# Kernel optimization log

Measured on AMD Instinct MI355X. Metric: run time of the kernel, lower is better.

Reference implementation:

```python
import jax, jax.numpy as jnp
import numpy as np

B, NQ, NV, DIM, HEADS, K = 2, 2048, 2048, 256, 8, 8
HD = DIM // HEADS
HID = 4 * DIM
SCALE = HD ** -0.5
EPS = 1e-5


def setup_inputs() -> dict:
    key = jax.random.key(0)
    ks = jax.random.split(key, 40)
    r = lambda i, s: jax.random.normal(ks[i], s, jnp.float32) * 0.02
    inp = {
        'q': jax.random.normal(ks[0], (B, NQ, DIM), jnp.float32),
        'v': jax.random.normal(ks[1], (B, NV, DIM), jnp.float32),
        'q_pos': jax.random.normal(ks[2], (B, NQ, 3), jnp.float32),
        'v_pos': jax.random.normal(ks[3], (B, NV, 3), jnp.float32),
        'self_knn_index': jax.random.randint(ks[4], (B, NQ, K), 0, NQ, jnp.int32),
        'cross_knn_index': jax.random.randint(ks[5], (B, NQ, K), 0, NV, jnp.int32),
        # LayerNorms (gamma=1, beta=0)
        'norm1_g': jnp.ones(DIM), 'norm1_b': jnp.zeros(DIM),
        'normq_g': jnp.ones(DIM), 'normq_b': jnp.zeros(DIM),
        'normv_g': jnp.ones(DIM), 'normv_b': jnp.zeros(DIM),
        'norm2_g': jnp.ones(DIM), 'norm2_b': jnp.zeros(DIM),
        # self-attention (qkv_bias=False), proj has bias
        'sa_qkv_w': r(6, (DIM, 3 * DIM)),
        'sa_proj_w': r(7, (DIM, DIM)), 'sa_proj_b': jnp.zeros(DIM),
        # cross-attention: q proj and kv proj (no bias), out proj with bias
        'ca_q_w': r(8, (DIM, DIM)),
        'ca_kv_w': r(9, (DIM, 2 * DIM)),
        'ca_proj_w': r(10, (DIM, DIM)), 'ca_proj_b': jnp.zeros(DIM),
        # MLP
        'fc1_w': r(11, (DIM, HID)), 'fc1_b': jnp.zeros(HID),
        'fc2_w': r(12, (HID, DIM)), 'fc2_b': jnp.zeros(DIM),
        # kNN maps
        'knn_w': r(13, (2 * DIM, DIM)), 'knn_b': jnp.zeros(DIM),
        'merge_w': r(14, (2 * DIM, DIM)), 'merge_b': jnp.zeros(DIM),
        'knnx_w': r(15, (2 * DIM, DIM)), 'knnx_b': jnp.zeros(DIM),
        'mergex_w': r(16, (2 * DIM, DIM)), 'mergex_b': jnp.zeros(DIM),
    }
    return inp


def _ln(x, g, b):
    m = x.mean(-1, keepdims=True)
    var = x.var(-1, keepdims=True)
    return (x - m) / jnp.sqrt(var + EPS) * g + b


def _heads(x):  # [B,N,DIM] -> [B,H,N,HD]
    Bx, N, _ = x.shape
    return x.reshape(Bx, N, HEADS, HD).transpose(0, 2, 1, 3)


def _attend(qh, kh, vh, proj_w, proj_b):
    a = jax.nn.softmax(jnp.einsum('bhqd,bhkd->bhqk', qh, kh) * SCALE, axis=-1)
    o = jnp.einsum('bhqk,bhkd->bhqd', a, vh)
    Bx, _, N, _ = o.shape
    o = o.transpose(0, 2, 1, 3).reshape(Bx, N, DIM)
    return o @ proj_w + proj_b


_gather = jax.vmap(lambda pts, idx: pts[idx])  # ([N,D],[Nq,K]) -> [Nq,K,D]


def _knn_feature(qn, vn, idx):  # gather -> diff/cat -> [B,Nq,K,2D]
    local = _gather(vn, idx)                      # [B,Nq,K,D]
    qe = qn[:, :, None, :]                        # [B,Nq,1,D]
    return jnp.concatenate([local - qe, jnp.broadcast_to(qe, local.shape)], -1)


def reference(q, v, q_pos, v_pos, self_knn_index, cross_knn_index,
              norm1_g, norm1_b, normq_g, normq_b, normv_g, normv_b,
              norm2_g, norm2_b, sa_qkv_w, sa_proj_w, sa_proj_b,
              ca_q_w, ca_kv_w, ca_proj_w, ca_proj_b,
              fc1_w, fc1_b, fc2_w, fc2_b,
              knn_w, knn_b, merge_w, merge_b,
              knnx_w, knnx_b, mergex_w, mergex_b):
    # ---- self-attention block with self-kNN branch ----
    nq = _ln(q, norm1_g, norm1_b)
    qkv = nq @ sa_qkv_w
    qh, kh, vh = (_heads(t) for t in jnp.split(qkv, 3, axis=-1))
    sa_out = _attend(qh, kh, vh, sa_proj_w, sa_proj_b)
    f = _knn_feature(nq, nq, self_knn_index)
    knn_out = jax.nn.leaky_relu(f @ knn_w + knn_b, 0.2).max(axis=-2)
    q1 = jnp.concatenate([sa_out, knn_out], -1) @ merge_w + merge_b
    q = q + q1
    # ---- cross-attention block with cross-kNN branch ----
    nq2 = _ln(q, normq_g, normq_b)
    nv = _ln(v, normv_g, normv_b)
    qh = _heads(nq2 @ ca_q_w)
    kh, vh = (_heads(t) for t in jnp.split(nv @ ca_kv_w, 2, axis=-1))
    ca_out = _attend(qh, kh, vh, ca_proj_w, ca_proj_b)
    f = _knn_feature(nq2, nv, cross_knn_index)
    knnx_out = jax.nn.leaky_relu(f @ knnx_w + knnx_b, 0.2).max(axis=-2)
    q2 = jnp.concatenate([ca_out, knnx_out], -1) @ mergex_w + mergex_b
    q = q + q2
    # ---- MLP block ----
    h = _ln(q, norm2_g, norm2_b)
    h = jax.nn.gelu(h @ fc1_w + fc1_b, approximate=False)
    q = q + (h @ fc2_w + fc2_b)
    return q
```

## Files before the change

### kernel.cpp

```cpp
#include <hip/hip_runtime.h>
#include <math.h>

#define NQC   2048
#define NKVC  2048
#define DIMC  256
#define SCALEF 0.2550348810731232f

typedef short bfrag __attribute__((ext_vector_type(8)));
typedef float ffrag __attribute__((ext_vector_type(4)));
typedef unsigned short us8 __attribute__((ext_vector_type(8)));

__device__ __forceinline__ float gelu_exact(float x) {
    return 0.5f * x * (1.0f + erff(x * 0.70710678118654752f));
}
__device__ __forceinline__ unsigned short f2bf(float f) {
    union { float f; unsigned u; } v; v.f = f;
    unsigned r = v.u + 0x7FFFu + ((v.u >> 16) & 1u);
    return (unsigned short)(r >> 16);
}
__device__ __forceinline__ float bf2f(unsigned short u) {
    union { unsigned u; float f; } v; v.u = ((unsigned)u) << 16;
    return v.f;
}
__device__ __forceinline__ float fexp2(float x) {
    float r; asm("v_exp_f32 %0, %1" : "=v"(r) : "v"(x)); return r;
}
__device__ __forceinline__ unsigned cvt_pk_bf16(float lo, float hi) {
    unsigned r; asm("v_cvt_pk_bf16_f32 %0, %1, %2" : "=v"(r) : "v"(lo), "v"(hi));
    return r;
}

__device__ __forceinline__ void ln_row(
    const float* __restrict__ x, const float* __restrict__ g,
    const float* __restrict__ b, unsigned short* __restrict__ y, int row)
{
    int lane = threadIdx.x & 63;
    const float* xr = x + (size_t)row * DIMC + lane * 4;
    float4 vv = *(const float4*)xr;
    float s  = vv.x + vv.y + vv.z + vv.w;
    float sq = vv.x*vv.x + vv.y*vv.y + vv.z*vv.z + vv.w*vv.w;
    #pragma unroll
    for (int off = 32; off >= 1; off >>= 1) {
        s  += __shfl_xor(s, off);
        sq += __shfl_xor(sq, off);
    }
    float mean = s * (1.0f/DIMC);
    float inv  = rsqrtf(sq * (1.0f/DIMC) - mean*mean + 1e-5f);
    float4 gg = *(const float4*)(g + lane*4);
    float4 bb = *(const float4*)(b + lane*4);
    ushort4 o;
    o.x = f2bf((vv.x - mean) * inv * gg.x + bb.x);
    o.y = f2bf((vv.y - mean) * inv * gg.y + bb.y);
    o.z = f2bf((vv.z - mean) * inv * gg.z + bb.z);
    o.w = f2bf((vv.w - mean) * inv * gg.w + bb.w);
    *(ushort4*)(y + (size_t)row * DIMC + lane * 4) = o;
}

__global__ __launch_bounds__(256) void prep_ln(
    const float* __restrict__ qkv, const float* __restrict__ knn,
    const float* __restrict__ proj, const float* __restrict__ merge,
    const float* __restrict__ caq, const float* __restrict__ knnx,
    const float* __restrict__ cakv, const float* __restrict__ projx,
    const float* __restrict__ mergex, const float* __restrict__ fc1,
    const float* __restrict__ fc2, unsigned short* __restrict__ dst,
    const float* __restrict__ lx, const float* __restrict__ lg,
    const float* __restrict__ lb, unsigned short* __restrict__ ly,
    const float* __restrict__ vx, const float* __restrict__ vg,
    const float* __restrict__ vb, unsigned short* __restrict__ vy,
    const float* __restrict__ pb1, const float* __restrict__ mb1, float* __restrict__ bf1o,
    const float* __restrict__ pbx, const float* __restrict__ mbx, float* __restrict__ bfxo)
{
    if (blockIdx.x >= 3584) {
        const float* bp = (blockIdx.x == 3584) ? pb1 : pbx;
        const float* Wm = (blockIdx.x == 3584) ? merge : mergex;
        const float* bm = (blockIdx.x == 3584) ? mb1 : mbx;
        float* o        = (blockIdx.x == 3584) ? bf1o : bfxo;
        int m = threadIdx.x;
        float acc = bm[m];
        for (int k = 0; k < 256; ++k) acc += bp[k] * Wm[(size_t)k * 256 + m];
        o[m] = acc;
        return;
    }
    if (blockIdx.x >= 2560) {
        int row = (blockIdx.x - 2560) * 4 + (threadIdx.x >> 6);
        ln_row(vx, vg, vb, vy, row);
        return;
    }
    if (blockIdx.x >= 1536) {
        int row = (blockIdx.x - 1536) * 4 + (threadIdx.x >> 6);
        ln_row(lx, lg, lb, ly, row);
        return;
    }
    int e = (blockIdx.x * 256 + threadIdx.x) * 4;
    float v[4];
    float scale = 1.0f;
    if (e < 327680) {
        int n = e >> 8, k = e & 255;
        if (n < 768) {
            const float* s = qkv + (size_t)k * 768 + n;
            #pragma unroll
            for (int i = 0; i < 4; ++i) v[i] = s[(size_t)i * 768];
            if (n < 256) scale = SCALEF;
        } else if (n < 1024) {
            const float* s = knn + (size_t)k * 256 + (n - 768);
            #pragma unroll
            for (int i = 0; i < 4; ++i) v[i] = s[(size_t)i * 256];
        } else {
            const float* s = knn + (size_t)k * 256 + (n - 1024);
            #pragma unroll
            for (int i = 0; i < 4; ++i) v[i] = s[65536 + (size_t)i * 256] - s[(size_t)i * 256];
        }
    } else if (e < 393216) {
        int l = e - 327680;
        const float* s = proj + l;
        #pragma unroll
        for (int i = 0; i < 4; ++i) v[i] = s[i];
    } else if (e < 524288) {
        int l = e - 393216, n = l >> 9, k = l & 511;
        const float* s = merge + (size_t)k * 256 + n;
        #pragma unroll
        for (int i = 0; i < 4; ++i) v[i] = s[(size_t)i * 256];
    } else if (e < 655360) {
        int l = e - 524288, n = l >> 8, k = l & 255;
        if (n < 256) {
            const float* s = caq + (size_t)k * 256 + n;
            #pragma unroll
            for (int i = 0; i < 4; ++i) v[i] = s[(size_t)i * 256];
            scale = SCALEF;
        } else {
            const float* s = knnx + (size_t)k * 256 + (n - 256);
            #pragma unroll
            for (int i = 0; i < 4; ++i) v[i] = s[65536 + (size_t)i * 256] - s[(size_t)i * 256];
        }
    } else if (e < 851968) {
        int l = e - 655360, n = l >> 8, k = l & 255;
        if (n < 512) {
            const float* s = cakv + (size_t)k * 512 + n;
            #pragma unroll
            for (int i = 0; i < 4; ++i) v[i] = s[(size_t)i * 512];
        } else {
            const float* s = knnx + (size_t)k * 256 + (n - 512);
            #pragma unroll
            for (int i = 0; i < 4; ++i) v[i] = s[(size_t)i * 256];
        }
    } else if (e < 917504) {
        int l = e - 851968;
        const float* s = projx + l;
        #pragma unroll
        for (int i = 0; i < 4; ++i) v[i] = s[i];
    } else if (e < 1048576) {
        int l = e - 917504, n = l >> 9, k = l & 511;
        const float* s = mergex + (size_t)k * 256 + n;
        #pragma unroll
        for (int i = 0; i < 4; ++i) v[i] = s[(size_t)i * 256];
    } else if (e < 1310720) {
        int l = e - 1048576, n = l >> 8, k = l & 255;
        const float* s = fc1 + (size_t)k * 1024 + n;
        #pragma unroll
        for (int i = 0; i < 4; ++i) v[i] = s[(size_t)i * 1024];
    } else {
        int l = e - 1310720, n = l >> 10, k = l & 1023;
        const float* s = fc2 + (size_t)k * 256 + n;
        #pragma unroll
        for (int i = 0; i < 4; ++i) v[i] = s[(size_t)i * 256];
    }
    ushort4 o;
    o.x = f2bf(v[0] * scale); o.y = f2bf(v[1] * scale);
    o.z = f2bf(v[2] * scale); o.w = f2bf(v[3] * scale);
    *(ushort4*)(dst + e) = o;
}

__global__ __launch_bounds__(256) void ln_b(
    const float* __restrict__ x, const float* __restrict__ g,
    const float* __restrict__ b, unsigned short* __restrict__ y)
{
    ln_row(x, g, b, y, blockIdx.x * 4 + (threadIdx.x >> 6));
}

template<int ACT, int RESID, int OUTBF, int VTM>
__device__ __forceinline__ void gemm_body(
    const unsigned short* __restrict__ A, int lda,
    const unsigned short* __restrict__ Wt,
    const float* __restrict__ bias,
    const float* __restrict__ resid, int ldr,
    void* __restrict__ Cp, int ldc, int Kc, int row0, int col0,
    unsigned short (* __restrict__ Alds)[72],
    unsigned short (* __restrict__ Wlds)[72],
    unsigned short* __restrict__ vt, int vlo)
{
    const int tid = threadIdx.x;
    const int wid = tid >> 6, lane = tid & 63;
    const int lm = lane & 15, quad = lane >> 4;
    const int wr = wid >> 1, wc = wid & 1;
    const int ar = tid >> 2, ac = (tid & 3) * 16;
    const unsigned short* Ag = A  + (size_t)(row0 + ar) * lda + ac;
    const unsigned short* Wg = Wt + (size_t)(col0 + ar) * Kc  + ac;

    us8 a0 = *(const us8*)Ag;
    us8 a1 = *(const us8*)(Ag + 8);
    us8 w0 = *(const us8*)Wg;
    us8 w1 = *(const us8*)(Wg + 8);

    ffrag acc[2][2];
    #pragma unroll
    for (int mi = 0; mi < 2; ++mi)
        #pragma unroll
        for (int ni = 0; ni < 2; ++ni)
            acc[mi][ni] = (ffrag){0.f, 0.f, 0.f, 0.f};

    for (int k0 = 0;;) {
        __syncthreads();
        *(us8*)&Alds[ar][ac]   = a0;
        *(us8*)&Alds[ar][ac+8] = a1;
        *(us8*)&Wlds[ar][ac]   = w0;
        *(us8*)&Wlds[ar][ac+8] = w1;
        __syncthreads();
        k0 += 64;
        if (k0 < Kc) {
            a0 = *(const us8*)(Ag + k0);
            a1 = *(const us8*)(Ag + k0 + 8);
            w0 = *(const us8*)(Wg + k0);
            w1 = *(const us8*)(Wg + k0 + 8);
        }
        #pragma unroll
        for (int kc = 0; kc < 2; ++kc) {
            bfrag af[2], bw[2];
            #pragma unroll
            for (int mi = 0; mi < 2; ++mi)
                af[mi] = *(const bfrag*)&Alds[wr*32 + mi*16 + lm][kc*32 + quad*8];
            #pragma unroll
            for (int ni = 0; ni < 2; ++ni)
                bw[ni] = *(const bfrag*)&Wlds[wc*32 + ni*16 + lm][kc*32 + quad*8];
            #pragma unroll
            for (int mi = 0; mi < 2; ++mi)
                #pragma unroll
                for (int ni = 0; ni < 2; ++ni)
                    acc[mi][ni] = __builtin_amdgcn_mfma_f32_16x16x32_bf16(
                        af[mi], bw[ni], acc[mi][ni], 0, 0, 0);
        }
        if (k0 >= Kc) break;
    }
    #pragma unroll
    for (int mi = 0; mi < 2; ++mi) {
        #pragma unroll
        for (int ni = 0; ni < 2; ++ni) {
            int gr = row0 + wr*32 + mi*16 + quad*4;
            int gc = col0 + wc*32 + ni*16 + lm;
            if (VTM && gc >= vlo && gc < vlo + 256) {
                int cv = gc - vlo, hh = cv >> 5, dd = cv & 31;
                int b = gr >> 11;
                int kin = gr & 63;
                int kblk = (gr & 2047) >> 6;
                int pos = ((kin & 15) << 2) | (kin >> 4);
                unsigned short* vp = vt + (((size_t)(b*8+hh)*32 + dd) * 2048)
                                       + kblk * 64 + pos;
                #pragma unroll
                for (int r = 0; r < 4; ++r)
                    vp[r * 4] = f2bf(acc[mi][ni][r]);
            } else {
                float bv = bias ? bias[gc] : 0.f;
                #pragma unroll
                for (int r = 0; r < 4; ++r) {
                    float o = acc[mi][ni][r] + bv;
                    if (ACT == 1) o = gelu_exact(o);
                    if (RESID) o += resid[(size_t)(gr + r) * ldr + gc];
                    if (OUTBF) ((unsigned short*)Cp)[(size_t)(gr + r) * ldc + gc] = f2bf(o);
                    else       ((float*)Cp)[(size_t)(gr + r) * ldc + gc] = o;
                }
            }
        }
    }
}

template<int ACT, int RESID, int OUTBF>
__global__ __launch_bounds__(256) void gemm64(
    const unsigned short* __restrict__ A, int lda,
    const unsigned short* __restrict__ Wt,
    const float* __restrict__ bias,
    const float* __restrict__ resid, int ldr,
    void* __restrict__ Cp, int ldc, int Kc)
{
    __shared__ unsigned short Alds[64][72];
    __shared__ unsigned short Wlds[64][72];
    gemm_body<ACT,RESID,OUTBF,0>(A, lda, Wt, bias, resid, ldr, Cp, ldc, Kc,
                                 blockIdx.y * 64, blockIdx.x * 64, Alds, Wlds,
                                 nullptr, 0);
}

__global__ __launch_bounds__(256) void gemm_qkv_fold(
    const unsigned short* __restrict__ XB, const unsigned short* __restrict__ WT1,
    unsigned short* __restrict__ A1,
    const unsigned short* __restrict__ WTmerge, const unsigned short* __restrict__ projbf,
    unsigned short* __restrict__ WTf1,
    const unsigned short* __restrict__ WTmergex, const unsigned short* __restrict__ projxbf,
    unsigned short* __restrict__ WTfx,
    unsigned short* __restrict__ VT)
{
    __shared__ unsigned short Alds[64][72];
    __shared__ unsigned short Wlds[64][72];
    const unsigned short *A, *Wt; unsigned short* C;
    int lda, ldc, row0, col0, vlo;
    if (blockIdx.y >= 64) {
        if (blockIdx.x >= 16) return;
        row0 = (blockIdx.x >> 2) * 64; col0 = (blockIdx.x & 3) * 64;
        lda = 512; ldc = 256; vlo = 1 << 30;
        if (blockIdx.y == 64) { A = WTmerge;  Wt = projbf;  C = WTf1; }
        else                  { A = WTmergex; Wt = projxbf; C = WTfx; }
    } else {
        A = XB; Wt = WT1; C = A1; lda = 256; ldc = 1280; vlo = 512;
        row0 = blockIdx.y * 64; col0 = blockIdx.x * 64;
    }
    gemm_body<0,0,1,1>(A, lda, Wt, nullptr, nullptr, 0, C, ldc, 256, row0, col0,
                       Alds, Wlds, VT, vlo);
}

template<int ACT, int RESID, int OUTBF>
__global__ __launch_bounds__(512) void gemm64x8(
    const unsigned short* __restrict__ A, int lda,
    const unsigned short* __restrict__ Wt,
    const float* __restrict__ bias,
    const float* __restrict__ resid, int ldr,
    void* __restrict__ Cp, int ldc, int Kc)
{
    __shared__ unsigned short Alds[2][64][72];
    __shared__ unsigned short Wlds[2][64][72];
    __shared__ float Red[64][68];
    const int tid = threadIdx.x;
    const int g = tid >> 8;
    const int t = tid & 255;
    const int wid2 = (tid >> 6) & 3, lane = tid & 63;
    const int lm = lane & 15, quad = lane >> 4;
    const int wr = wid2 >> 1, wc = wid2 & 1;
    const int row0 = blockIdx.y * 64, col0 = blockIdx.x * 64;
    const int ar = t >> 2, ac = (t & 3) * 16;
    const int KH = Kc >> 1;
    const unsigned short* Ag = A  + (size_t)(row0 + ar) * lda + g * KH + ac;
    const unsigned short* Wg = Wt + (size_t)(col0 + ar) * Kc  + g * KH + ac;

    us8 a0 = *(const us8*)Ag;
    us8 a1 = *(const us8*)(Ag + 8);
    us8 w0 = *(const us8*)Wg;
    us8 w1 = *(const us8*)(Wg + 8);

    ffrag acc[2][2];
    #pragma unroll
    for (int mi = 0; mi < 2; ++mi)
        #pragma unroll
        for (int ni = 0; ni < 2; ++ni)
            acc[mi][ni] = (ffrag){0.f, 0.f, 0.f, 0.f};

    for (int k0 = 0;;) {
        __syncthreads();
        *(us8*)&Alds[g][ar][ac]   = a0;
        *(us8*)&Alds[g][ar][ac+8] = a1;
        *(us8*)&Wlds[g][ar][ac]   = w0;
        *(us8*)&Wlds[g][ar][ac+8] = w1;
        __syncthreads();
        k0 += 64;
        if (k0 < KH) {
            a0 = *(const us8*)(Ag + k0);
            a1 = *(const us8*)(Ag + k0 + 8);
            w0 = *(const us8*)(Wg + k0);
            w1 = *(const us8*)(Wg + k0 + 8);
        }
        #pragma unroll
        for (int kc = 0; kc < 2; ++kc) {
            bfrag af[2], bw[2];
            #pragma unroll
            for (int mi = 0; mi < 2; ++mi)
                af[mi] = *(const bfrag*)&Alds[g][wr*32 + mi*16 + lm][kc*32 + quad*8];
            #pragma unroll
            for (int ni = 0; ni < 2; ++ni)
                bw[ni] = *(const bfrag*)&Wlds[g][wc*32 + ni*16 + lm][kc*32 + quad*8];
            #pragma unroll
            for (int mi = 0; mi < 2; ++mi)
                #pragma unroll
                for (int ni = 0; ni < 2; ++ni)
                    acc[mi][ni] = __builtin_amdgcn_mfma_f32_16x16x32_bf16(
                        af[mi], bw[ni], acc[mi][ni], 0, 0, 0);
        }
        if (k0 >= KH) break;
    }
    __syncthreads();
    if (g == 1) {
        #pragma unroll
        for (int mi = 0; mi < 2; ++mi)
            #pragma unroll
            for (int ni = 0; ni < 2; ++ni) {
                int lr = wr*32 + mi*16 + quad*4;
                int lc = wc*32 + ni*16 + lm;
                #pragma unroll
                for (int r = 0; r < 4; ++r)
                    Red[lr + r][lc] = acc[mi][ni][r];
            }
    }
    __syncthreads();
    if (g == 0) {
        #pragma unroll
        for (int mi = 0; mi < 2; ++mi) {
            #pragma unroll
            for (int ni = 0; ni < 2; ++ni) {
                int lr = wr*32 + mi*16 + quad*4;
                int lc = wc*32 + ni*16 + lm;
                int gr = row0 + lr;
                int gc = col0 + lc;
                float bv = bias ? bias[gc] : 0.f;
                #pragma unroll
                for (int r = 0; r < 4; ++r) {
                    float o = acc[mi][ni][r] + Red[lr + r][lc] + bv;
                    if (ACT == 1) o = gelu_exact(o);
                    if (RESID) o += resid[(size_t)(gr + r) * ldr + gc];
                    if (OUTBF) ((unsigned short*)Cp)[(size_t)(gr + r) * ldc + gc] = f2bf(o);
                    else       ((float*)Cp)[(size_t)(gr + r) * ldc + gc] = o;
                }
            }
        }
    }
}

__global__ __launch_bounds__(512) void gemm64x8f(
    const unsigned short* __restrict__ O,
    const unsigned short* __restrict__ Akn,
    const unsigned short* __restrict__ W0,
    const unsigned short* __restrict__ W1,
    const float* __restrict__ bias,
    const float* __restrict__ resid,
    float* __restrict__ Cp)
{
    __shared__ unsigned short Alds[2][64][72];
    __shared__ unsigned short Wlds[2][64][72];
    __shared__ float Red[64][68];
    const int tid = threadIdx.x;
    const int g = tid >> 8;
    const int t = tid & 255;
    const int wid2 = (tid >> 6) & 3, lane = tid & 63;
    const int lm = lane & 15, quad = lane >> 4;
    const int wr = wid2 >> 1, wc = wid2 & 1;
    const int row0 = blockIdx.y * 64, col0 = blockIdx.x * 64;
    const int ar = t >> 2, ac = (t & 3) * 16;
    const int grow = row0 + ar;

    const unsigned short* Ag = g ? Akn + (size_t)grow * 512 + ac
                                 : O   + (size_t)grow * 256 + ac;
    const unsigned short* Wg = g ? W1 + (size_t)(col0 + ar) * 512 + ac
                                 : W0 + (size_t)(col0 + ar) * 256 + ac;

    us8 a0 = *(const us8*)Ag;
    us8 a1 = *(const us8*)(Ag + 8);
    us8 w0 = *(const us8*)Wg;
    us8 w1 = *(const us8*)(Wg + 8);

    ffrag acc[2][2];
    #pragma unroll
    for (int mi = 0; mi < 2; ++mi)
        #pragma unroll
        for (int ni = 0; ni < 2; ++ni)
            acc[mi][ni] = (ffrag){0.f, 0.f, 0.f, 0.f};

    for (int k0 = 0;;) {
        __syncthreads();
        *(us8*)&Alds[g][ar][ac]   = a0;
        *(us8*)&Alds[g][ar][ac+8] = a1;
        *(us8*)&Wlds[g][ar][ac]   = w0;
        *(us8*)&Wlds[g][ar][ac+8] = w1;
        __syncthreads();
        k0 += 64;
        if (k0 < 256) {
            a0 = *(const us8*)(Ag + k0);
            a1 = *(const us8*)(Ag + k0 + 8);
            w0 = *(const us8*)(Wg + k0);
            w1 = *(const us8*)(Wg + k0 + 8);
        }
        #pragma unroll
        for (int kc = 0; kc < 2; ++kc) {
            bfrag af[2], bw[2];
            #pragma unroll
            for (int mi = 0; mi < 2; ++mi)
                af[mi] = *(const bfrag*)&Alds[g][wr*32 + mi*16 + lm][kc*32 + quad*8];
            #pragma unroll
            for (int ni = 0; ni < 2; ++ni)
                bw[ni] = *(const bfrag*)&Wlds[g][wc*32 + ni*16 + lm][kc*32 + quad*8];
            #pragma unroll
            for (int mi = 0; mi < 2; ++mi)
                #pragma unroll
                for (int ni = 0; ni < 2; ++ni)
                    acc[mi][ni] = __builtin_amdgcn_mfma_f32_16x16x32_bf16(
                        af[mi], bw[ni], acc[mi][ni], 0, 0, 0);
        }
        if (k0 >= 256) break;
    }
    __syncthreads();
    if (g == 1) {
        #pragma unroll
        for (int mi = 0; mi < 2; ++mi)
            #pragma unroll
            for (int ni = 0; ni < 2; ++ni) {
                int lr = wr*32 + mi*16 + quad*4;
                int lc = wc*32 + ni*16 + lm;
                #pragma unroll
                for (int r = 0; r < 4; ++r)
                    Red[lr + r][lc] = acc[mi][ni][r];
            }
    }
    __syncthreads();
    if (g == 0) {
        #pragma unroll
        for (int mi = 0; mi < 2; ++mi) {
            #pragma unroll
            for (int ni = 0; ni < 2; ++ni) {
                int lr = wr*32 + mi*16 + quad*4;
                int lc = wc*32 + ni*16 + lm;
                int gr = row0 + lr;
                int gc = col0 + lc;
                float bv = bias[gc];
                #pragma unroll
                for (int r = 0; r < 4; ++r)
                    Cp[(size_t)(gr + r) * 256 + gc] =
                        acc[mi][ni][r] + Red[lr + r][lc] + bv
                        + resid[(size_t)(gr + r) * 256 + gc];
            }
        }
    }
}

__global__ __launch_bounds__(256) void gemm64_dual(
    const unsigned short* __restrict__ XB,
    const unsigned short* __restrict__ NVB,
    const unsigned short* __restrict__ WT2,
    const unsigned short* __restrict__ WT3,
    unsigned short* __restrict__ A2,
    unsigned short* __restrict__ A3,
    unsigned short* __restrict__ VT)
{
    __shared__ unsigned short Alds[64][72];
    __shared__ unsigned short Wlds[64][72];
    const unsigned short* A; const unsigned short* Wt;
    unsigned short* C; int ldc, col0, vlo;
    if (blockIdx.x < 8) { A = XB;  Wt = WT2; C = A2; ldc = 512; col0 = blockIdx.x * 64; vlo = 1 << 30; }
    else                { A = NVB; Wt = WT3; C = A3; ldc = 768; col0 = (blockIdx.x - 8) * 64; vlo = 256; }
    gemm_body<0,0,1,1>(A, 256, Wt, nullptr, nullptr, 0, C, ldc, 256,
                       blockIdx.y * 64, col0, Alds, Wlds, VT, vlo);
}

__global__ __launch_bounds__(256) void attn_gather(
    const unsigned short* __restrict__ Qp, int ldq,
    const unsigned short* __restrict__ Kp, int ldk,
    const unsigned short* __restrict__ VT,
    unsigned short* __restrict__ Op,
    const unsigned short* __restrict__ P, int ldp,
    const unsigned short* __restrict__ Base, int ldb,
    const float* __restrict__ gbias, const int* __restrict__ idx,
    unsigned short* __restrict__ gout, int ldgo)
{
    __shared__ unsigned short Klds[64][40];
    __shared__ __align__(16) unsigned short Vt[32][72];
    __shared__ __align__(16) unsigned short Plds[4][2][16][72];
    int tid = threadIdx.x, wid = tid >> 6, lane = tid & 63;

    if (blockIdx.z >= 1) {
        int gbid = blockIdx.x + 32 * (blockIdx.y + 8 * (blockIdx.z - 1));
        int q = gbid * 4 + wid;
        int b = q >> 11;
        int c = lane * 4;
        ushort4 bu = *(const ushort4*)(Base + (size_t)q * ldb + c);
        float4 bi = *(const float4*)(gbias + c);
        float bsx = bf2f(bu.x) + bi.x, bsy = bf2f(bu.y) + bi.y;
        float bsz = bf2f(bu.z) + bi.z, bsw = bf2f(bu.w) + bi.w;
        float4 acc = make_float4(-3e38f, -3e38f, -3e38f, -3e38f);
        const int* ip = idx + (size_t)q * 8;
        #pragma unroll
        for (int k = 0; k < 8; ++k) {
            int j = ip[k];
            ushort4 pu = *(const ushort4*)(P + ((size_t)(b * NKVC + j)) * ldp + c);
            float t;
            t = bsx + bf2f(pu.x); t = t > 0.f ? t : 0.2f * t; acc.x = fmaxf(acc.x, t);
            t = bsy + bf2f(pu.y); t = t > 0.f ? t : 0.2f * t; acc.y = fmaxf(acc.y, t);
            t = bsz + bf2f(pu.z); t = t > 0.f ? t : 0.2f * t; acc.z = fmaxf(acc.z, t);
            t = bsw + bf2f(pu.w); t = t > 0.f ? t : 0.2f * t; acc.w = fmaxf(acc.w, t);
        }
        ushort4 o;
        o.x = f2bf(acc.x); o.y = f2bf(acc.y); o.z = f2bf(acc.z); o.w = f2bf(acc.w);
        *(ushort4*)(gout + (size_t)q * ldgo + c) = o;
        return;
    }

    int bb = blockIdx.x >> 4, qc = blockIdx.x & 15;
    int h = blockIdx.y;
    int hoff = h * 32;
    int lm = lane & 15, quad = lane >> 4;
    size_t qbase  = (size_t)bb * NQC;
    size_t kvbase = (size_t)bb * NKVC;
    int q0 = qc * 128 + wid * 32;

    bfrag aq0 = *(const bfrag*)(Qp + (qbase + q0 + lm)      * (size_t)ldq + hoff + quad * 8);
    bfrag aq1 = *(const bfrag*)(Qp + (qbase + q0 + 16 + lm) * (size_t)ldq + hoff + quad * 8);

    float l0[4] = {0.f, 0.f, 0.f, 0.f};
    float l1[4] = {0.f, 0.f, 0.f, 0.f};
    ffrag oacc[2][2];
    #pragma unroll
    for (int i = 0; i < 2; ++i)
        #pragma unroll
        for (int j = 0; j < 2; ++j)
            oacc[i][j] = (ffrag){0.f, 0.f, 0.f, 0.f};

    const int kkey = tid >> 2, kd0 = (tid & 3) * 8;
    const int vrow = tid >> 3, vp0 = (tid & 7) * 8;
    const unsigned short* kg0 = Kp + (kvbase + kkey) * (size_t)ldk + hoff + kd0;
    const unsigned short* vg0 = VT + (((size_t)bb * 8 + h) * 32 + vrow) * 2048 + vp0;

    for (int kt = 0; kt < 32; ++kt) {
        us8 kv = *(const us8*)(kg0 + (size_t)kt * 64 * ldk);
        us8 vv = *(const us8*)(vg0 + kt * 64);
        __syncthreads();
        *(us8*)&Klds[kkey][kd0] = kv;
        *(us8*)&Vt[vrow][vp0]   = vv;
        __syncthreads();

        ffrag s0[4], s1[4];
        #pragma unroll
        for (int t = 0; t < 4; ++t) {
            bfrag bk = *(const bfrag*)&Klds[t*16 + lm][quad * 8];
            s0[t] = __builtin_amdgcn_mfma_f32_16x16x32_bf16(
                aq0, bk, (ffrag){0.f,0.f,0.f,0.f}, 0, 0, 0);
            s1[t] = __builtin_amdgcn_mfma_f32_16x16x32_bf16(
                aq1, bk, (ffrag){0.f,0.f,0.f,0.f}, 0, 0, 0);
        }

        #pragma unroll
        for (int r = 0; r < 4; ++r) {
            float p0 = fexp2(s0[0][r]), p1 = fexp2(s0[1][r]);
            float p2 = fexp2(s0[2][r]), p3 = fexp2(s0[3][r]);
            l0[r] += (p0 + p1) + (p2 + p3);
            *(uint2*)&Plds[wid][0][quad*4 + r][lm << 2] =
                make_uint2(cvt_pk_bf16(p0, p1), cvt_pk_bf16(p2, p3));
            float u0 = fexp2(s1[0][r]), u1 = fexp2(s1[1][r]);
            float u2 = fexp2(s1[2][r]), u3 = fexp2(s1[3][r]);
            l1[r] += (u0 + u1) + (u2 + u3);
            *(uint2*)&Plds[wid][1][quad*4 + r][lm << 2] =
                make_uint2(cvt_pk_bf16(u0, u1), cvt_pk_bf16(u2, u3));
        }
        asm volatile("s_waitcnt lgkmcnt(0)" ::: "memory");

        #pragma unroll
        for (int kc = 0; kc < 2; ++kc) {
            bfrag bv0 = *(const bfrag*)&Vt[lm][kc*32 + quad*8];
            bfrag bv1 = *(const bfrag*)&Vt[16 + lm][kc*32 + quad*8];
            bfrag ap0 = *(const bfrag*)&Plds[wid][0][lm][kc*32 + quad*8];
            bfrag ap1 = *(const bfrag*)&Plds[wid][1][lm][kc*32 + quad*8];
            oacc[0][0] = __builtin_amdgcn_mfma_f32_16x16x32_bf16(ap0, bv0, oacc[0][0], 0, 0, 0);
            oacc[0][1] = __builtin_amdgcn_mfma_f32_16x16x32_bf16(ap0, bv1, oacc[0][1], 0, 0, 0);
            oacc[1][0] = __builtin_amdgcn_mfma_f32_16x16x32_bf16(ap1, bv0, oacc[1][0], 0, 0, 0);
            oacc[1][1] = __builtin_amdgcn_mfma_f32_16x16x32_bf16(ap1, bv1, oacc[1][1], 0, 0, 0);
        }
    }
    #pragma unroll
    for (int r = 0; r < 4; ++r) {
        float a = l0[r], b = l1[r];
        a += __shfl_xor(a, 1); a += __shfl_xor(a, 2);
        a += __shfl_xor(a, 4); a += __shfl_xor(a, 8);
        b += __shfl_xor(b, 1); b += __shfl_xor(b, 2);
        b += __shfl_xor(b, 4); b += __shfl_xor(b, 8);
        l0[r] = 1.0f / a; l1[r] = 1.0f / b;
    }
    #pragma unroll
    for (int nt = 0; nt < 2; ++nt)
        #pragma unroll
        for (int r = 0; r < 4; ++r) {
            Op[(qbase + q0 + quad*4 + r) * 256 + hoff + nt*16 + lm]
                = f2bf(oacc[0][nt][r] * l0[r]);
            Op[(qbase + q0 + 16 + quad*4 + r) * 256 + hoff + nt*16 + lm]
                = f2bf(oacc[1][nt][r] * l1[r]);
        }
}

extern "C" void kernel_launch(void* const* d_in, const int* in_sizes, int n_in,
                              void* d_out, int out_size, void* d_ws, size_t ws_size,
                              hipStream_t stream) {
    const float* q_in   = (const float*)d_in[0];
    const float* v_in   = (const float*)d_in[1];
    const int*   idx_s  = (const int*)d_in[4];
    const int*   idx_x  = (const int*)d_in[5];
    const float* n1g = (const float*)d_in[6],  *n1b = (const float*)d_in[7];
    const float* nqg = (const float*)d_in[8],  *nqb = (const float*)d_in[9];
    const float* nvg = (const float*)d_in[10], *nvb = (const float*)d_in[11];
    const float* n2g = (const float*)d_in[12], *n2b = (const float*)d_in[13];
    const float* sa_qkv_w  = (const float*)d_in[14];
    const float* sa_proj_w = (const float*)d_in[15];
    const float* sa_proj_b = (const float*)d_in[16];
    const float* ca_q_w    = (const float*)d_in[17];
    const float* ca_kv_w   = (const float*)d_in[18];
    const float* ca_proj_w = (const float*)d_in[19];
    const float* ca_proj_b = (const float*)d_in[20];
    const float* fc1_w = (const float*)d_in[21], *fc1_b = (const float*)d_in[22];
    const float* fc2_w = (const float*)d_in[23], *fc2_b = (const float*)d_in[24];
    const float* knn_w   = (const float*)d_in[25], *knn_b   = (const float*)d_in[26];
    const float* merge_w = (const float*)d_in[27], *merge_b = (const float*)d_in[28];
    const float* knnx_w  = (const float*)d_in[29], *knnx_b  = (const float*)d_in[30];
    const float* mergex_w = (const float*)d_in[31], *mergex_b = (const float*)d_in[32];
    float* out = (float*)d_out;

    unsigned short* A1      = (unsigned short*)d_ws;
    unsigned short* A2      = A1;
    unsigned short* A3      = A1 + (size_t)4096 * 512;
    unsigned short* Hb      = A1;
    unsigned short* KN      = A1 + (size_t)4096 * 1280;
    unsigned short* CC      = KN;
    unsigned short* XB      = CC + (size_t)4096 * 512;
    unsigned short* NVB     = XB + (size_t)4096 * 256;
    unsigned short* WT      = NVB + (size_t)4096 * 256;
    unsigned short* WT1     = WT;
    unsigned short* projbf  = WT + 327680;
    unsigned short* WTmerge = WT + 393216;
    unsigned short* WT2     = WT + 524288;
    unsigned short* WT3     = WT + 655360;
    unsigned short* projxbf = WT + 851968;
    unsigned short* WTmergex= WT + 917504;
    unsigned short* WTfc1   = WT + 1048576;
    unsigned short* WTfc2   = WT + 1310720;
    unsigned short* Opart   = WT + 1572864;
    unsigned short* WTf1    = Opart + (size_t)4096 * 256;
    unsigned short* WTfx    = WTf1 + 65536;
    float* bf1 = (float*)(WTfx + 65536);
    float* bfx = bf1 + 256;
    unsigned short* VT = (unsigned short*)(bfx + 256);

    dim3 blk(256), blk8(512);
    dim3 gAG(32, 8, 5);

    prep_ln<<<dim3(3586), blk, 0, stream>>>(sa_qkv_w, knn_w, sa_proj_w, merge_w,
        ca_q_w, knnx_w, ca_kv_w, ca_proj_w, mergex_w, fc1_w, fc2_w, WT,
        q_in, n1g, n1b, XB,
        v_in, nvg, nvb, NVB,
        sa_proj_b, merge_b, bf1,
        ca_proj_b, mergex_b, bfx);

    gemm_qkv_fold<<<dim3(20,66), blk, 0, stream>>>(XB, WT1, A1,
        WTmerge, projbf, WTf1, WTmergex, projxbf, WTfx, VT);
    attn_gather<<<gAG, blk, 0, stream>>>(A1, 1280, A1+256, 1280, VT,
        Opart, A1+768, 1280, A1+1024, 1280, knn_b, idx_s, CC+256, 512);
    gemm64x8f<<<dim3(4,64), blk8, 0, stream>>>(Opart, CC+256,
        WTf1, WTmerge+256, bf1, q_in, out);

    ln_b<<<dim3(1024), blk, 0, stream>>>(out, nqg, nqb, XB);
    gemm64_dual<<<dim3(20,64), blk, 0, stream>>>(XB, NVB, WT2, WT3, A2, A3, VT);
    attn_gather<<<gAG, blk, 0, stream>>>(A2, 512, A3, 768, VT,
        Opart, A3+512, 768, A2+256, 512, knnx_b, idx_x, CC+256, 512);
    gemm64x8f<<<dim3(4,64), blk8, 0, stream>>>(Opart, CC+256,
        WTfx, WTmergex+256, bfx, out, out);

    ln_b<<<dim3(1024), blk, 0, stream>>>(out, n2g, n2b, XB);
    gemm64<1,0,1><<<dim3(16,64), blk, 0, stream>>>(XB, 256, WTfc1,
        fc1_b, nullptr, 0, Hb, 1024, 256);
    gemm64x8<0,1,0><<<dim3(4,64), blk8, 0, stream>>>(Hb, 1024, WTfc2,
        fc2_b, out, 256, out, 256, 1024);
}
```

Baseline: 263.6 us.

## Halve attention query tile per wave and stage V-transpose writes through LDS

The attention kernel now gives each wave 16 queries instead of 32. This doubles the attention grid to 64 blocks in x, and the gather section's z dimension shrinks to 3 so it keeps the same total block count. The aim is more parallelism and lower register pressure, at the cost of loading each K/V tile twice as often across blocks. Separately, the GEMM epilogue that writes the transposed V layout now stages the tile in LDS and emits 16-byte vector stores, replacing scattered 2-byte global writes.

```diff
diff --git a/kernel.cpp b/kernel.cpp
--- a/kernel.cpp
+++ b/kernel.cpp
@@ -240,33 +240,45 @@
         }
         if (k0 >= Kc) break;
     }
+    if (VTM && col0 >= vlo && col0 - vlo < 256) {
+        __syncthreads();
+        #pragma unroll
+        for (int mi = 0; mi < 2; ++mi) {
+            #pragma unroll
+            for (int ni = 0; ni < 2; ++ni) {
+                int lr = wr*32 + mi*16 + quad*4;
+                int lc = wc*32 + ni*16 + lm;
+                #pragma unroll
+                for (int r = 0; r < 4; ++r) {
+                    int k = lr + r;
+                    Alds[lc][((k & 15) << 2) | (k >> 4)] = f2bf(acc[mi][ni][r]);
+                }
+            }
+        }
+        __syncthreads();
+        int d = tid >> 2, p0 = (tid & 3) * 16;
+        int cv = col0 - vlo + d, hh = cv >> 5, dd = cv & 31;
+        int bq = row0 >> 11, kblk = (row0 & 2047) >> 6;
+        unsigned short* vp = vt + (((size_t)(bq * 8 + hh) * 32 + dd) * 2048)
+                                + kblk * 64 + p0;
+        *(us8*)vp       = *(const us8*)&Alds[d][p0];
+        *(us8*)(vp + 8) = *(const us8*)&Alds[d][p0 + 8];
+        return;
+    }
     #pragma unroll
     for (int mi = 0; mi < 2; ++mi) {
         #pragma unroll
         for (int ni = 0; ni < 2; ++ni) {
             int gr = row0 + wr*32 + mi*16 + quad*4;
             int gc = col0 + wc*32 + ni*16 + lm;
-            if (VTM && gc >= vlo && gc < vlo + 256) {
-                int cv = gc - vlo, hh = cv >> 5, dd = cv & 31;
-                int b = gr >> 11;
-                int kin = gr & 63;
-                int kblk = (gr & 2047) >> 6;
-                int pos = ((kin & 15) << 2) | (kin >> 4);
-                unsigned short* vp = vt + (((size_t)(b*8+hh)*32 + dd) * 2048)
-                                       + kblk * 64 + pos;
-                #pragma unroll
-                for (int r = 0; r < 4; ++r)
-                    vp[r * 4] = f2bf(acc[mi][ni][r]);
-            } else {
-                float bv = bias ? bias[gc] : 0.f;
-                #pragma unroll
-                for (int r = 0; r < 4; ++r) {
-                    float o = acc[mi][ni][r] + bv;
-                    if (ACT == 1) o = gelu_exact(o);
-                    if (RESID) o += resid[(size_t)(gr + r) * ldr + gc];
-                    if (OUTBF) ((unsigned short*)Cp)[(size_t)(gr + r) * ldc + gc] = f2bf(o);
-                    else       ((float*)Cp)[(size_t)(gr + r) * ldc + gc] = o;
-                }
+            float bv = bias ? bias[gc] : 0.f;
+            #pragma unroll
+            for (int r = 0; r < 4; ++r) {
+                float o = acc[mi][ni][r] + bv;
+                if (ACT == 1) o = gelu_exact(o);
+                if (RESID) o += resid[(size_t)(gr + r) * ldr + gc];
+                if (OUTBF) ((unsigned short*)Cp)[(size_t)(gr + r) * ldc + gc] = f2bf(o);
+                else       ((float*)Cp)[(size_t)(gr + r) * ldc + gc] = o;
             }
         }
     }
@@ -554,11 +566,11 @@
 {
     __shared__ unsigned short Klds[64][40];
     __shared__ __align__(16) unsigned short Vt[32][72];
-    __shared__ __align__(16) unsigned short Plds[4][2][16][72];
+    __shared__ __align__(16) unsigned short Plds[4][16][72];
     int tid = threadIdx.x, wid = tid >> 6, lane = tid & 63;
 
     if (blockIdx.z >= 1) {
-        int gbid = blockIdx.x + 32 * (blockIdx.y + 8 * (blockIdx.z - 1));
+        int gbid = blockIdx.x + 64 * (blockIdx.y + 8 * (blockIdx.z - 1));
         int q = gbid * 4 + wid;
         int b = q >> 11;
         int c = lane * 4;
@@ -584,25 +596,20 @@
         return;
     }
 
-    int bb = blockIdx.x >> 4, qc = blockIdx.x & 15;
+    int bb = blockIdx.x >> 5, qc = blockIdx.x & 31;
     int h = blockIdx.y;
     int hoff = h * 32;
     int lm = lane & 15, quad = lane >> 4;
     size_t qbase  = (size_t)bb * NQC;
     size_t kvbase = (size_t)bb * NKVC;
-    int q0 = qc * 128 + wid * 32;
-
-    bfrag aq0 = *(const bfrag*)(Qp + (qbase + q0 + lm)      * (size_t)ldq + hoff + quad * 8);
-    bfrag aq1 = *(const bfrag*)(Qp + (qbase + q0 + 16 + lm) * (size_t)ldq + hoff + quad * 8);
-
-    float l0[4] = {0.f, 0.f, 0.f, 0.f};
-    float l1[4] = {0.f, 0.f, 0.f, 0.f};
-    ffrag oacc[2][2];
-    #pragma unroll
-    for (int i = 0; i < 2; ++i)
-        #pragma unroll
-        for (int j = 0; j < 2; ++j)
-            oacc[i][j] = (ffrag){0.f, 0.f, 0.f, 0.f};
+    int q0 = qc * 64 + wid * 16;
+
+    bfrag aq = *(const bfrag*)(Qp + (qbase + q0 + lm) * (size_t)ldq + hoff + quad * 8);
+
+    float l_r[4] = {0.f, 0.f, 0.f, 0.f};
+    ffrag oacc[2];
+    oacc[0] = (ffrag){0.f, 0.f, 0.f, 0.f};
+    oacc[1] = (ffrag){0.f, 0.f, 0.f, 0.f};
 
     const int kkey = tid >> 2, kd0 = (tid & 3) * 8;
     const int vrow = tid >> 3, vp0 = (tid & 7) * 8;
@@ -617,61 +624,46 @@
         *(us8*)&Vt[vrow][vp0]   = vv;
         __syncthreads();
 
-        ffrag s0[4], s1[4];
+        ffrag sacc[4];
         #pragma unroll
         for (int t = 0; t < 4; ++t) {
             bfrag bk = *(const bfrag*)&Klds[t*16 + lm][quad * 8];
-            s0[t] = __builtin_amdgcn_mfma_f32_16x16x32_bf16(
-                aq0, bk, (ffrag){0.f,0.f,0.f,0.f}, 0, 0, 0);
-            s1[t] = __builtin_amdgcn_mfma_f32_16x16x32_bf16(
-                aq1, bk, (ffrag){0.f,0.f,0.f,0.f}, 0, 0, 0);
+            sacc[t] = __builtin_amdgcn_mfma_f32_16x16x32_bf16(
+                aq, bk, (ffrag){0.f,0.f,0.f,0.f}, 0, 0, 0);
         }
 
         #pragma unroll
         for (int r = 0; r < 4; ++r) {
-            float p0 = fexp2(s0[0][r]), p1 = fexp2(s0[1][r]);
-            float p2 = fexp2(s0[2][r]), p3 = fexp2(s0[3][r]);
-            l0[r] += (p0 + p1) + (p2 + p3);
-            *(uint2*)&Plds[wid][0][quad*4 + r][lm << 2] =
+            float p0 = fexp2(sacc[0][r]), p1 = fexp2(sacc[1][r]);
+            float p2 = fexp2(sacc[2][r]), p3 = fexp2(sacc[3][r]);
+            l_r[r] += (p0 + p1) + (p2 + p3);
+            *(uint2*)&Plds[wid][quad*4 + r][lm << 2] =
                 make_uint2(cvt_pk_bf16(p0, p1), cvt_pk_bf16(p2, p3));
-            float u0 = fexp2(s1[0][r]), u1 = fexp2(s1[1][r]);
-            float u2 = fexp2(s1[2][r]), u3 = fexp2(s1[3][r]);
-            l1[r] += (u0 + u1) + (u2 + u3);
-            *(uint2*)&Plds[wid][1][quad*4 + r][lm << 2] =
-                make_uint2(cvt_pk_bf16(u0, u1), cvt_pk_bf16(u2, u3));
         }
         asm volatile("s_waitcnt lgkmcnt(0)" ::: "memory");
 
         #pragma unroll
         for (int kc = 0; kc < 2; ++kc) {
+            bfrag ap  = *(const bfrag*)&Plds[wid][lm][kc*32 + quad*8];
             bfrag bv0 = *(const bfrag*)&Vt[lm][kc*32 + quad*8];
             bfrag bv1 = *(const bfrag*)&Vt[16 + lm][kc*32 + quad*8];
-            bfrag ap0 = *(const bfrag*)&Plds[wid][0][lm][kc*32 + quad*8];
-            bfrag ap1 = *(const bfrag*)&Plds[wid][1][lm][kc*32 + quad*8];
-            oacc[0][0] = __builtin_amdgcn_mfma_f32_16x16x32_bf16(ap0, bv0, oacc[0][0], 0, 0, 0);
-            oacc[0][1] = __builtin_amdgcn_mfma_f32_16x16x32_bf16(ap0, bv1, oacc[0][1], 0, 0, 0);
-            oacc[1][0] = __builtin_amdgcn_mfma_f32_16x16x32_bf16(ap1, bv0, oacc[1][0], 0, 0, 0);
-            oacc[1][1] = __builtin_amdgcn_mfma_f32_16x16x32_bf16(ap1, bv1, oacc[1][1], 0, 0, 0);
+            oacc[0] = __builtin_amdgcn_mfma_f32_16x16x32_bf16(ap, bv0, oacc[0], 0, 0, 0);
+            oacc[1] = __builtin_amdgcn_mfma_f32_16x16x32_bf16(ap, bv1, oacc[1], 0, 0, 0);
         }
     }
     #pragma unroll
     for (int r = 0; r < 4; ++r) {
-        float a = l0[r], b = l1[r];
+        float a = l_r[r];
         a += __shfl_xor(a, 1); a += __shfl_xor(a, 2);
         a += __shfl_xor(a, 4); a += __shfl_xor(a, 8);
-        b += __shfl_xor(b, 1); b += __shfl_xor(b, 2);
-        b += __shfl_xor(b, 4); b += __shfl_xor(b, 8);
-        l0[r] = 1.0f / a; l1[r] = 1.0f / b;
+        l_r[r] = 1.0f / a;
     }
     #pragma unroll
     for (int nt = 0; nt < 2; ++nt)
         #pragma unroll
-        for (int r = 0; r < 4; ++r) {
+        for (int r = 0; r < 4; ++r)
             Op[(qbase + q0 + quad*4 + r) * 256 + hoff + nt*16 + lm]
-                = f2bf(oacc[0][nt][r] * l0[r]);
-            Op[(qbase + q0 + 16 + quad*4 + r) * 256 + hoff + nt*16 + lm]
-                = f2bf(oacc[1][nt][r] * l1[r]);
-        }
+                = f2bf(oacc[nt][r] * l_r[r]);
 }
 
 extern "C" void kernel_launch(void* const* d_in, const int* in_sizes, int n_in,
@@ -726,7 +718,7 @@
     unsigned short* VT = (unsigned short*)(bfx + 256);
 
     dim3 blk(256), blk8(512);
-    dim3 gAG(32, 8, 5);
+    dim3 gAG(64, 8, 3);
 
     prep_ln<<<dim3(3586), blk, 0, stream>>>(sa_qkv_w, knn_w, sa_proj_w, merge_w,
         ca_q_w, knnx_w, ca_kv_w, ca_proj_w, mergex_w, fc1_w, fc2_w, WT,
```

After: 248.3 us. -5.8%, faster.
